# Kernel optimization log

Measured on AMD Instinct MI355X. Metric: run time of the kernel, lower is better.

The kernel has to match this reference:

```python
import jax, jax.numpy as jnp
import numpy as np

EPS = 1e-5      # F.layer_norm default eps
ALPHA = 0.08    # ALALLaDA blend coefficient


def setup_inputs() -> dict:
    key = jax.random.key(0)
    ks = jax.random.split(key, 6)
    B, S, D, K = 2, 2048, 2048, 8
    Fh = D // 4
    h_L = jax.random.normal(ks[0], (B, S, D), jnp.float32)
    # nonzero -> masked position (stands in for input_ids == 126336)
    mask = jax.random.randint(ks[1], (B, S), 0, 2).astype(jnp.int32)
    Wr = jax.random.normal(ks[2], (K, D), jnp.float32) / np.sqrt(D).astype(np.float32)
    br = jnp.zeros((K,), jnp.float32)
    W1 = jax.random.normal(ks[3], (K, D, Fh), jnp.float32) / np.sqrt(D).astype(np.float32)
    b1 = jnp.zeros((K, Fh), jnp.float32)
    W2 = jax.random.normal(ks[4], (K, Fh, D), jnp.float32) / np.sqrt(Fh).astype(np.float32)
    b2 = jnp.zeros((K, D), jnp.float32)
    return {"h_L": h_L, "mask": mask, "Wr": Wr, "br": br,
            "W1": W1, "b1": b1, "W2": W2, "b2": b2, "range_r": 8}


def _router_blend(h_L, Wr, br, W1, b1, W2, b2, mask, range_r):
    B, S, D = h_L.shape
    masked = mask != 0
    um = (~masked).astype(h_L.dtype)  # unmasked validity [B,S]
    # Per-token, per-expert outputs M[b,s,k,d]: Linear -> exact GELU -> Linear.
    pre = jnp.einsum('bsd,kdf->bskf', h_L, W1) + b1
    M = jnp.einsum('bskf,kfd->bskd', jax.nn.gelu(pre, approximate=False), W2) + b2
    # Routing weights at every position (softmax over K experts).
    w = jax.nn.softmax(jnp.einsum('bsd,kd->bsk', h_L, Wr) + br, axis=-1)
    # Accumulate weighted expert outputs over the +/-range_r neighbor window,
    # counting only unmasked neighbors. Fixed small loop over 2r offsets.
    num = jnp.zeros((B, S, D), h_L.dtype)
    cnt = jnp.zeros((B, S), h_L.dtype)
    for o in range(-range_r, range_r + 1):
        if o == 0:
            continue
        if o > 0:  # neighbor t = a + o: shift left, zero-pad tail
            Mo = jnp.pad(M[:, o:], ((0, 0), (0, o), (0, 0), (0, 0)))
            vo = jnp.pad(um[:, o:], ((0, 0), (0, o)))
        else:      # neighbor t = a + o (o<0): shift right, zero-pad head
            Mo = jnp.pad(M[:, :o], ((0, 0), (-o, 0), (0, 0), (0, 0)))
            vo = jnp.pad(um[:, :o], ((0, 0), (-o, 0)))
        num = num + vo[..., None] * jnp.einsum('bsk,bskd->bsd', w, Mo)
        cnt = cnt + vo
    has = cnt > 0
    mean = num / jnp.maximum(cnt, 1.0)[..., None]   # mean over valid neighbors
    # layer_norm over d_model, no affine
    mu = mean.mean(-1, keepdims=True)
    var = jnp.mean((mean - mu) ** 2, axis=-1, keepdims=True)
    ln = (mean - mu) / jnp.sqrt(var + EPS)
    # delta is written only at masked positions that had >=1 neighbor
    delta = jnp.where((masked & has)[..., None], ln, 0.0)
    return h_L + ALPHA * delta


def reference(h_L, mask, Wr, br, W1, b1, W2, b2, range_r):
    return _router_blend(h_L, Wr, br, W1, b1, W2, b2, mask, range_r)
```

## Files before the change

### kernel.cpp

```cpp
#include <hip/hip_runtime.h>
#include <hip/hip_bf16.h>
#include <math.h>


#define ALPHA 0.08f
#define EPS 1e-5f

typedef __attribute__((ext_vector_type(8))) __bf16 bf16x8;
typedef __attribute__((ext_vector_type(8))) short short8;
typedef __attribute__((ext_vector_type(4))) float f32x4;

__device__ __forceinline__ unsigned short f2bf(float f) {
  unsigned u = __float_as_uint(f);
  u += 0x7fffu + ((u >> 16) & 1u);
  return (unsigned short)(u >> 16);
}
__device__ __forceinline__ float bf2f(unsigned short b) {
  return __uint_as_float(((unsigned)b) << 16);
}

#define GLD16(gptr, lptr)                                                     \
  __builtin_amdgcn_global_load_lds(                                           \
      (const __attribute__((address_space(1))) void*)(gptr),                  \
      (__attribute__((address_space(3))) void*)(lptr), 16, 0, 0)

__device__ __forceinline__ int wave_incl_scan(int v, int lane) {
#pragma unroll
  for (int off = 1; off < 64; off <<= 1) {
    int t = __shfl_up(v, off);
    if (lane >= off) v += t;
  }
  return v;
}

__global__ __launch_bounds__(1024) void scan_kernel(
    const int* __restrict__ mask, const int* __restrict__ rptr,
    int* __restrict__ ru, int* __restrict__ unm_idx,
    int* __restrict__ msk_idx, int* __restrict__ pos2row,
    int* __restrict__ counts) {
  __shared__ int sru[4097];
  __shared__ int wsum[16];
  __shared__ int wsum2[17];
  const int tid = threadIdx.x;
  const int lane = tid & 63, wv = tid >> 6;
  const int t0 = tid * 4;
  const int4 m4 = *(const int4*)(mask + t0);
  int f[4];
  f[0] = (m4.x == 0); f[1] = (m4.y == 0); f[2] = (m4.z == 0); f[3] = (m4.w == 0);
  const int tsum = f[0] + f[1] + f[2] + f[3];
  const int isc = wave_incl_scan(tsum, lane);
  if (lane == 63) wsum[wv] = isc;
  __syncthreads();
  if (tid == 0) {
    int acc = 0;
#pragma unroll
    for (int i = 0; i < 16; ++i) { int v = wsum[i]; wsum[i] = acc; acc += v; }
    sru[4096] = acc;
    counts[0] = acc;
    ru[4096] = acc;
  }
  __syncthreads();
  int ex = wsum[wv] + isc - tsum;
#pragma unroll
  for (int j = 0; j < 4; ++j) {
    sru[t0 + j] = ex;
    ru[t0 + j] = ex;
    if (f[j]) unm_idx[ex] = t0 + j;
    ex += f[j];
  }
  __syncthreads();
  const int r = rptr[0];
  int mval[4] = {m4.x, m4.y, m4.z, m4.w};
  int g[4];
#pragma unroll
  for (int j = 0; j < 4; ++j) {
    const int t = t0 + j;
    const int s = t & 2047, tb = t & ~2047;
    const int lo = max(s - r, 0), hi = min(s + r, 2047);
    const int cnt = sru[tb + hi + 1] - sru[tb + lo];
    g[j] = (mval[j] != 0 && cnt > 0) ? 1 : 0;
  }
  const int tsum2 = g[0] + g[1] + g[2] + g[3];
  const int isc2 = wave_incl_scan(tsum2, lane);
  if (lane == 63) wsum2[wv] = isc2;
  __syncthreads();
  if (tid == 0) {
    int acc = 0;
#pragma unroll
    for (int i = 0; i < 16; ++i) { int v = wsum2[i]; wsum2[i] = acc; acc += v; }
    counts[1] = acc;
  }
  __syncthreads();
  int ex2 = wsum2[wv] + isc2 - tsum2;
#pragma unroll
  for (int j = 0; j < 4; ++j) {
    const int t = t0 + j;
    pos2row[t] = g[j] ? ex2 : -1;
    if (g[j]) msk_idx[ex2] = t;
    ex2 += g[j];
  }
}

__global__ void pack_h_kernel(const float* __restrict__ h,
                              const int* __restrict__ unm_idx,
                              const int* __restrict__ counts,
                              unsigned short* __restrict__ hbc) {
  const int i = blockIdx.x;
  if (i >= counts[0]) return;
  const int t = unm_idx[i];
  const int d0 = threadIdx.x * 8;
  const float4 x0 = *(const float4*)(h + (size_t)t * 2048 + d0);
  const float4 x1 = *(const float4*)(h + (size_t)t * 2048 + d0 + 4);
  short8 o;
  o[0] = (short)f2bf(x0.x); o[1] = (short)f2bf(x0.y);
  o[2] = (short)f2bf(x0.z); o[3] = (short)f2bf(x0.w);
  o[4] = (short)f2bf(x1.x); o[5] = (short)f2bf(x1.y);
  o[6] = (short)f2bf(x1.z); o[7] = (short)f2bf(x1.w);
  *(short8*)(hbc + (size_t)i * 2048 + d0) = o;
}

__global__ void transpose_pack_kernel(const float* __restrict__ src,
                                      unsigned short* __restrict__ dst,
                                      int R, int C, size_t dstStride,
                                      size_t dstExpStride) {
  __shared__ float tile[32][33];
  const int k = blockIdx.z;
  src += (size_t)k * (size_t)R * (size_t)C;
  dst += (size_t)k * dstExpStride;
  const int c0 = blockIdx.x * 32;
  const int r0 = blockIdx.y * 32;
  const int tx = threadIdx.x;
  const int ty = threadIdx.y;
#pragma unroll
  for (int i = 0; i < 4; ++i)
    tile[ty + 8 * i][tx] = src[(size_t)(r0 + ty + 8 * i) * C + (c0 + tx)];
  __syncthreads();
#pragma unroll
  for (int i = 0; i < 4; ++i) {
    const int c = c0 + ty + 8 * i;
    dst[(size_t)c * dstStride + (size_t)(r0 + tx)] = f2bf(tile[tx][ty + 8 * i]);
  }
}

__global__ void router_kernel(const float* __restrict__ h,
                              const float* __restrict__ Wr,
                              const float* __restrict__ br,
                              float* __restrict__ w) {
  const int a = blockIdx.x;
  const int tid = threadIdx.x;
  const int lane = tid & 63, wid = tid >> 6;
  const size_t base = (size_t)a * 2048;
  const int d0 = tid * 8;
  float hv[8];
  *(float4*)(hv) = *(const float4*)(h + base + d0);
  *(float4*)(hv + 4) = *(const float4*)(h + base + d0 + 4);
  float acc[8];
#pragma unroll
  for (int k = 0; k < 8; ++k) {
    float wvv[8];
    *(float4*)(wvv) = *(const float4*)(Wr + (size_t)k * 2048 + d0);
    *(float4*)(wvv + 4) = *(const float4*)(Wr + (size_t)k * 2048 + d0 + 4);
    float s = 0.f;
#pragma unroll
    for (int j = 0; j < 8; ++j) s += hv[j] * wvv[j];
    acc[k] = s;
  }
#pragma unroll
  for (int off = 32; off > 0; off >>= 1)
#pragma unroll
    for (int k = 0; k < 8; ++k) acc[k] += __shfl_down(acc[k], off);
  __shared__ float red[4][8];
  __shared__ float logits[8];
  if (lane == 0)
#pragma unroll
    for (int k = 0; k < 8; ++k) red[wid][k] = acc[k];
  __syncthreads();
  if (tid < 8)
    logits[tid] = red[0][tid] + red[1][tid] + red[2][tid] + red[3][tid] + br[tid];
  __syncthreads();
  if (tid == 0) {
    float mx = logits[0];
#pragma unroll
    for (int k = 1; k < 8; ++k) mx = fmaxf(mx, logits[k]);
    float e[8], se = 0.f;
#pragma unroll
    for (int k = 0; k < 8; ++k) {
      e[k] = expf(logits[k] - mx);
      se += e[k];
    }
    const float is = 1.f / se;
#pragma unroll
    for (int k = 0; k < 8; ++k) w[(size_t)a * 8 + k] = e[k] * is;
  }
}

template <int EPI>
__global__ __launch_bounds__(256, 2) void gemm_bt_kernel(
    const unsigned short* __restrict__ A, const unsigned short* __restrict__ Bt,
    float* __restrict__ Cf, unsigned short* __restrict__ Cb,
    const float* __restrict__ bias, const int* __restrict__ counts, int cidx,
    int N, int Kd) {
  const int Mlim = counts[cidx];
  const int bm = blockIdx.y * 128;
  if (bm >= Mlim) return;
  __shared__ __align__(16) unsigned short As[4096];
  __shared__ __align__(16) unsigned short Bs[4096];
  const int tid = threadIdx.x;
  const int lane = tid & 63;
  const int wid = tid >> 6;
  const int bn = blockIdx.x * 128;
  const int wr = wid >> 1;
  const int wc = wid & 1;

  f32x4 acc[4][4];
#pragma unroll
  for (int m = 0; m < 4; ++m)
#pragma unroll
    for (int n = 0; n < 4; ++n) acc[m][n] = (f32x4){0.f, 0.f, 0.f, 0.f};

  const int srow = wid * 16 + (lane >> 2);
  const int scol = (lane & 3) * 8;
  const unsigned short* gA0 = A + (size_t)(bm + srow) * Kd + scol;
  const unsigned short* gA1 = gA0 + (size_t)64 * Kd;
  const unsigned short* gB0 = Bt + (size_t)(bn + srow) * Kd + scol;
  const unsigned short* gB1 = gB0 + (size_t)64 * Kd;
  unsigned short* lA0 = As + wid * 512;
  unsigned short* lA1 = As + (wid + 4) * 512;
  unsigned short* lB0 = Bs + wid * 512;
  unsigned short* lB1 = Bs + (wid + 4) * 512;

  const int aoff = (wr * 64 + (lane & 15)) * 32 + (lane >> 4) * 8;
  const int boff = (wc * 64 + (lane & 15)) * 32 + (lane >> 4) * 8;

  for (int k0 = 0; k0 < Kd; k0 += 32) {
    __syncthreads();
    GLD16(gA0 + k0, lA0);
    GLD16(gA1 + k0, lA1);
    GLD16(gB0 + k0, lB0);
    GLD16(gB1 + k0, lB1);
    __syncthreads();
    bf16x8 af[4], bfr[4];
#pragma unroll
    for (int m = 0; m < 4; ++m)
      af[m] = __builtin_bit_cast(bf16x8, *(const short8*)(As + aoff + m * 512));
#pragma unroll
    for (int n = 0; n < 4; ++n)
      bfr[n] = __builtin_bit_cast(bf16x8, *(const short8*)(Bs + boff + n * 512));
#pragma unroll
    for (int m = 0; m < 4; ++m)
#pragma unroll
      for (int n = 0; n < 4; ++n)
        acc[m][n] = __builtin_amdgcn_mfma_f32_16x16x32_bf16(af[m], bfr[n],
                                                            acc[m][n], 0, 0, 0);
  }

  const int r0 = bm + wr * 64 + (lane >> 4) * 4;
  const int c0 = bn + wc * 64 + (lane & 15);
#pragma unroll
  for (int m = 0; m < 4; ++m) {
#pragma unroll
    for (int n = 0; n < 4; ++n) {
      const int col = c0 + n * 16;
#pragma unroll
      for (int i = 0; i < 4; ++i) {
        const int row = r0 + m * 16 + i;
        if (row >= Mlim) continue;
        const size_t off = (size_t)row * N + col;
        float v = acc[m][n][i];
        if (EPI == 1) {
          v += bias[col];
          v = 0.5f * v * (1.0f + erff(v * 0.70710678118654752f));
          Cb[off] = f2bf(v);
        } else {
          Cf[off] = v;
        }
      }
    }
  }
}

__global__ void window_kernel(const unsigned short* __restrict__ Act_c,
                              const float* __restrict__ w,
                              const int* __restrict__ msk_idx,
                              const int* __restrict__ ru,
                              const int* __restrict__ rptr,
                              const int* __restrict__ counts,
                              unsigned short* __restrict__ G_c) {
  const int i = blockIdx.y;
  if (i >= counts[1]) return;
  const int a = msk_idx[i];
  const int s = a & 2047;
  const int tb = a & ~2047;
  const int r = rptr[0];
  const int lo = max(s - r, 0), hi = min(s + r, 2047);
  const int jlo = ru[tb + lo], jhi = ru[tb + hi + 1];
  const int c = blockIdx.x * 2048 + threadIdx.x * 8;
  float acc[8] = {0.f, 0.f, 0.f, 0.f, 0.f, 0.f, 0.f, 0.f};
  for (int j = jlo; j < jhi; ++j) {
    const short8 v = *(const short8*)(Act_c + (size_t)j * 4096 + c);
#pragma unroll
    for (int jj = 0; jj < 8; ++jj) acc[jj] += bf2f((unsigned short)v[jj]);
  }
  const float wv = w[(size_t)a * 8 + (c >> 9)];
  short8 o8;
#pragma unroll
  for (int jj = 0; jj < 8; ++jj) o8[jj] = (short)f2bf(acc[jj] * wv);
  *(short8*)(G_c + (size_t)i * 4096 + c) = o8;
}

__global__ void final_kernel(const float* __restrict__ h,
                             const int* __restrict__ pos2row,
                             const float* __restrict__ w,
                             const float* __restrict__ b2,
                             const float* __restrict__ num_c,
                             const int* __restrict__ ru,
                             const int* __restrict__ rptr,
                             float* __restrict__ out) {
  const int a = blockIdx.x;
  const int tid = threadIdx.x;
  const int lane = tid & 63, wid = tid >> 6;
  const size_t base = (size_t)a * 2048;
  const int d0 = tid * 8;
  const int row = pos2row[a];
  if (row < 0) {
    const float4 x0 = *(const float4*)(h + base + d0);
    const float4 x1 = *(const float4*)(h + base + d0 + 4);
    *(float4*)(out + base + d0) = x0;
    *(float4*)(out + base + d0 + 4) = x1;
    return;
  }
  const int s = a & 2047;
  const int tb = a & ~2047;
  const int r = rptr[0];
  const int lo = max(s - r, 0), hi = min(s + r, 2047);
  const int cnt = ru[tb + hi + 1] - ru[tb + lo];
  float wk[8];
#pragma unroll
  for (int k = 0; k < 8; ++k) wk[k] = w[(size_t)a * 8 + k];
  const float cntf = (float)cnt;
  const float icnt = 1.0f / cntf;
  float mval[8];
  float s1 = 0.f, s2 = 0.f;
#pragma unroll
  for (int j = 0; j < 8; ++j) {
    const int d = d0 + j;
    float wb2 = 0.f;
#pragma unroll
    for (int k = 0; k < 8; ++k) wb2 += wk[k] * b2[(size_t)k * 2048 + d];
    const float v = (num_c[(size_t)row * 2048 + d] + cntf * wb2) * icnt;
    mval[j] = v;
    s1 += v;
    s2 += v * v;
  }
#pragma unroll
  for (int off = 32; off > 0; off >>= 1) {
    s1 += __shfl_down(s1, off);
    s2 += __shfl_down(s2, off);
  }
  __shared__ float red[8];
  if (lane == 0) {
    red[wid] = s1;
    red[4 + wid] = s2;
  }
  __syncthreads();
  const float S1 = red[0] + red[1] + red[2] + red[3];
  const float S2 = red[4] + red[5] + red[6] + red[7];
  const float mu = S1 * (1.0f / 2048.0f);
  const float var = S2 * (1.0f / 2048.0f) - mu * mu;
  const float rin = rsqrtf(var + EPS);
#pragma unroll
  for (int j = 0; j < 8; ++j) {
    const int d = d0 + j;
    out[base + d] = h[base + d] + ALPHA * ((mval[j] - mu) * rin);
  }
}

extern "C" void kernel_launch(void* const* d_in, const int* in_sizes, int n_in,
                              void* d_out, int out_size, void* d_ws,
                              size_t ws_size, hipStream_t stream) {
  const float* h = (const float*)d_in[0];
  const int* mask = (const int*)d_in[1];
  const float* Wr = (const float*)d_in[2];
  const float* br = (const float*)d_in[3];
  const float* W1 = (const float*)d_in[4];
  const float* b1 = (const float*)d_in[5];
  const float* W2 = (const float*)d_in[6];
  const float* b2 = (const float*)d_in[7];
  const int* rptr = (const int*)d_in[8];
  float* out = (float*)d_out;

  char* ws = (char*)d_ws;
  unsigned short* hbc = (unsigned short*)(ws + 0);
  unsigned short* B1t = (unsigned short*)(ws + 16777216);
  unsigned short* B2t = (unsigned short*)(ws + 33554432);
  unsigned short* Act_c = (unsigned short*)(ws + 50331648);
  unsigned short* G_c = (unsigned short*)(ws + 83886080);
  float* num_c = (float*)(ws + 50331648);
  float* wbuf = (float*)(ws + 117440512);
  int* ru = (int*)(ws + 117571584);
  int* unm_idx = ru + 4100;
  int* msk_idx = unm_idx + 4096;
  int* pos2row = msk_idx + 4096;
  int* counts = pos2row + 4096;

  scan_kernel<<<1, 1024, 0, stream>>>(mask, rptr, ru, unm_idx, msk_idx,
                                      pos2row, counts);
  pack_h_kernel<<<4096, 256, 0, stream>>>(h, unm_idx, counts, hbc);
  router_kernel<<<4096, 256, 0, stream>>>(h, Wr, br, wbuf);
  transpose_pack_kernel<<<dim3(16, 64, 8), dim3(32, 8), 0, stream>>>(
      W1, B1t, 2048, 512, 2048, (size_t)512 * 2048);
  transpose_pack_kernel<<<dim3(64, 16, 8), dim3(32, 8), 0, stream>>>(
      W2, B2t, 512, 2048, 4096, 512);
  gemm_bt_kernel<1><<<dim3(32, 32), 256, 0, stream>>>(
      hbc, B1t, nullptr, Act_c, b1, counts, 0, 4096, 2048);
  window_kernel<<<dim3(2, 4096), 256, 0, stream>>>(Act_c, wbuf, msk_idx, ru,
                                                   rptr, counts, G_c);
  gemm_bt_kernel<0><<<dim3(16, 32), 256, 0, stream>>>(
      G_c, B2t, num_c, nullptr, nullptr, counts, 1, 2048, 4096);
  final_kernel<<<4096, 256, 0, stream>>>(h, pos2row, wbuf, b2, num_c, ru,
                                         rptr, out);
}
```

Before: 375.5 us.

## Multi-buffer GEMM LDS loads with 4-stage pipeline and fuse pack with router

The GEMM main loop moves from a single LDS buffer with two barriers per k-step to a 4-deep ring of buffers. Three stages are prefetched with global_load_lds, and explicit vmcnt waits let loads overlap MFMA compute. Separately, the bf16 packing of unmasked rows is merged into the router kernel so h is read once instead of twice, saving one launch. LDS per block grows to 64KB, which may limit occupancy relative to the launch_bounds(256,2) target.

New measurement: 346.7 us. 7.6% less time.

```diff
diff --git a/kernel.cpp b/kernel.cpp
--- a/kernel.cpp
+++ b/kernel.cpp
@@ -101,22 +101,66 @@
   }
 }
 
-__global__ void pack_h_kernel(const float* __restrict__ h,
-                              const int* __restrict__ unm_idx,
-                              const int* __restrict__ counts,
-                              unsigned short* __restrict__ hbc) {
-  const int i = blockIdx.x;
-  if (i >= counts[0]) return;
-  const int t = unm_idx[i];
-  const int d0 = threadIdx.x * 8;
-  const float4 x0 = *(const float4*)(h + (size_t)t * 2048 + d0);
-  const float4 x1 = *(const float4*)(h + (size_t)t * 2048 + d0 + 4);
-  short8 o;
-  o[0] = (short)f2bf(x0.x); o[1] = (short)f2bf(x0.y);
-  o[2] = (short)f2bf(x0.z); o[3] = (short)f2bf(x0.w);
-  o[4] = (short)f2bf(x1.x); o[5] = (short)f2bf(x1.y);
-  o[6] = (short)f2bf(x1.z); o[7] = (short)f2bf(x1.w);
-  *(short8*)(hbc + (size_t)i * 2048 + d0) = o;
+__global__ void packrouter_kernel(const float* __restrict__ h,
+                                  const int* __restrict__ mask,
+                                  const int* __restrict__ ru,
+                                  const float* __restrict__ Wr,
+                                  const float* __restrict__ br,
+                                  float* __restrict__ w,
+                                  unsigned short* __restrict__ hbc) {
+  const int a = blockIdx.x;
+  const int tid = threadIdx.x;
+  const int lane = tid & 63, wid = tid >> 6;
+  const size_t base = (size_t)a * 2048;
+  const int d0 = tid * 8;
+  float hv[8];
+  *(float4*)(hv) = *(const float4*)(h + base + d0);
+  *(float4*)(hv + 4) = *(const float4*)(h + base + d0 + 4);
+  float acc[8];
+#pragma unroll
+  for (int k = 0; k < 8; ++k) {
+    float wvv[8];
+    *(float4*)(wvv) = *(const float4*)(Wr + (size_t)k * 2048 + d0);
+    *(float4*)(wvv + 4) = *(const float4*)(Wr + (size_t)k * 2048 + d0 + 4);
+    float s = 0.f;
+#pragma unroll
+    for (int j = 0; j < 8; ++j) s += hv[j] * wvv[j];
+    acc[k] = s;
+  }
+#pragma unroll
+  for (int off = 32; off > 0; off >>= 1)
+#pragma unroll
+    for (int k = 0; k < 8; ++k) acc[k] += __shfl_down(acc[k], off);
+  __shared__ float red[4][8];
+  __shared__ float logits[8];
+  if (lane == 0)
+#pragma unroll
+    for (int k = 0; k < 8; ++k) red[wid][k] = acc[k];
+  __syncthreads();
+  if (tid < 8)
+    logits[tid] = red[0][tid] + red[1][tid] + red[2][tid] + red[3][tid] + br[tid];
+  __syncthreads();
+  if (tid == 0) {
+    float mx = logits[0];
+#pragma unroll
+    for (int k = 1; k < 8; ++k) mx = fmaxf(mx, logits[k]);
+    float e[8], se = 0.f;
+#pragma unroll
+    for (int k = 0; k < 8; ++k) {
+      e[k] = expf(logits[k] - mx);
+      se += e[k];
+    }
+    const float is = 1.f / se;
+#pragma unroll
+    for (int k = 0; k < 8; ++k) w[(size_t)a * 8 + k] = e[k] * is;
+  }
+  if (mask[a] == 0) {
+    const int i = ru[a];
+    short8 o;
+#pragma unroll
+    for (int j = 0; j < 8; ++j) o[j] = (short)f2bf(hv[j]);
+    *(short8*)(hbc + (size_t)i * 2048 + d0) = o;
+  }
 }
 
 __global__ void transpose_pack_kernel(const float* __restrict__ src,
@@ -142,58 +186,6 @@
   }
 }
 
-__global__ void router_kernel(const float* __restrict__ h,
-                              const float* __restrict__ Wr,
-                              const float* __restrict__ br,
-                              float* __restrict__ w) {
-  const int a = blockIdx.x;
-  const int tid = threadIdx.x;
-  const int lane = tid & 63, wid = tid >> 6;
-  const size_t base = (size_t)a * 2048;
-  const int d0 = tid * 8;
-  float hv[8];
-  *(float4*)(hv) = *(const float4*)(h + base + d0);
-  *(float4*)(hv + 4) = *(const float4*)(h + base + d0 + 4);
-  float acc[8];
-#pragma unroll
-  for (int k = 0; k < 8; ++k) {
-    float wvv[8];
-    *(float4*)(wvv) = *(const float4*)(Wr + (size_t)k * 2048 + d0);
-    *(float4*)(wvv + 4) = *(const float4*)(Wr + (size_t)k * 2048 + d0 + 4);
-    float s = 0.f;
-#pragma unroll
-    for (int j = 0; j < 8; ++j) s += hv[j] * wvv[j];
-    acc[k] = s;
-  }
-#pragma unroll
-  for (int off = 32; off > 0; off >>= 1)
-#pragma unroll
-    for (int k = 0; k < 8; ++k) acc[k] += __shfl_down(acc[k], off);
-  __shared__ float red[4][8];
-  __shared__ float logits[8];
-  if (lane == 0)
-#pragma unroll
-    for (int k = 0; k < 8; ++k) red[wid][k] = acc[k];
-  __syncthreads();
-  if (tid < 8)
-    logits[tid] = red[0][tid] + red[1][tid] + red[2][tid] + red[3][tid] + br[tid];
-  __syncthreads();
-  if (tid == 0) {
-    float mx = logits[0];
-#pragma unroll
-    for (int k = 1; k < 8; ++k) mx = fmaxf(mx, logits[k]);
-    float e[8], se = 0.f;
-#pragma unroll
-    for (int k = 0; k < 8; ++k) {
-      e[k] = expf(logits[k] - mx);
-      se += e[k];
-    }
-    const float is = 1.f / se;
-#pragma unroll
-    for (int k = 0; k < 8; ++k) w[(size_t)a * 8 + k] = e[k] * is;
-  }
-}
-
 template <int EPI>
 __global__ __launch_bounds__(256, 2) void gemm_bt_kernel(
     const unsigned short* __restrict__ A, const unsigned short* __restrict__ Bt,
@@ -203,8 +195,7 @@
   const int Mlim = counts[cidx];
   const int bm = blockIdx.y * 128;
   if (bm >= Mlim) return;
-  __shared__ __align__(16) unsigned short As[4096];
-  __shared__ __align__(16) unsigned short Bs[4096];
+  __shared__ __align__(16) unsigned short L[4][8192];
   const int tid = threadIdx.x;
   const int lane = tid & 63;
   const int wid = tid >> 6;
@@ -224,35 +215,68 @@
   const unsigned short* gA1 = gA0 + (size_t)64 * Kd;
   const unsigned short* gB0 = Bt + (size_t)(bn + srow) * Kd + scol;
   const unsigned short* gB1 = gB0 + (size_t)64 * Kd;
-  unsigned short* lA0 = As + wid * 512;
-  unsigned short* lA1 = As + (wid + 4) * 512;
-  unsigned short* lB0 = Bs + wid * 512;
-  unsigned short* lB1 = Bs + (wid + 4) * 512;
 
   const int aoff = (wr * 64 + (lane & 15)) * 32 + (lane >> 4) * 8;
   const int boff = (wc * 64 + (lane & 15)) * 32 + (lane >> 4) * 8;
 
-  for (int k0 = 0; k0 < Kd; k0 += 32) {
-    __syncthreads();
-    GLD16(gA0 + k0, lA0);
-    GLD16(gA1 + k0, lA1);
-    GLD16(gB0 + k0, lB0);
-    GLD16(gB1 + k0, lB1);
-    __syncthreads();
-    bf16x8 af[4], bfr[4];
-#pragma unroll
-    for (int m = 0; m < 4; ++m)
-      af[m] = __builtin_bit_cast(bf16x8, *(const short8*)(As + aoff + m * 512));
-#pragma unroll
-    for (int n = 0; n < 4; ++n)
-      bfr[n] = __builtin_bit_cast(bf16x8, *(const short8*)(Bs + boff + n * 512));
-#pragma unroll
-    for (int m = 0; m < 4; ++m)
-#pragma unroll
-      for (int n = 0; n < 4; ++n)
-        acc[m][n] = __builtin_amdgcn_mfma_f32_16x16x32_bf16(af[m], bfr[n],
-                                                            acc[m][n], 0, 0, 0);
-  }
+#define STAGE(buf, t)                                                         \
+  {                                                                           \
+    const int k0_ = (t) << 5;                                                 \
+    unsigned short* la_ = &L[(buf)][0] + wid * 512;                           \
+    unsigned short* lb_ = &L[(buf)][4096] + wid * 512;                        \
+    GLD16(gA0 + k0_, la_);                                                    \
+    GLD16(gA1 + k0_, la_ + 2048);                                             \
+    GLD16(gB0 + k0_, lb_);                                                    \
+    GLD16(gB1 + k0_, lb_ + 2048);                                             \
+  }
+
+#define COMPUTE(buf)                                                          \
+  {                                                                           \
+    const unsigned short* As_ = &L[(buf)][0];                                 \
+    const unsigned short* Bs_ = &L[(buf)][4096];                              \
+    bf16x8 af[4], bfr[4];                                                     \
+    _Pragma("unroll") for (int m = 0; m < 4; ++m) af[m] =                     \
+        __builtin_bit_cast(bf16x8, *(const short8*)(As_ + aoff + m * 512));   \
+    _Pragma("unroll") for (int n = 0; n < 4; ++n) bfr[n] =                    \
+        __builtin_bit_cast(bf16x8, *(const short8*)(Bs_ + boff + n * 512));   \
+    _Pragma("unroll") for (int m = 0; m < 4; ++m)                             \
+        _Pragma("unroll") for (int n = 0; n < 4; ++n) acc[m][n] =             \
+            __builtin_amdgcn_mfma_f32_16x16x32_bf16(af[m], bfr[n],            \
+                                                    acc[m][n], 0, 0, 0);      \
+  }
+
+  const int nt = Kd >> 5;
+  STAGE(0, 0);
+  STAGE(1, 1);
+  STAGE(2, 2);
+#pragma unroll 1
+  for (int t = 0; t < nt - 3; ++t) {
+    asm volatile("s_waitcnt vmcnt(8)" ::: "memory");
+    __builtin_amdgcn_s_barrier();
+    __builtin_amdgcn_sched_barrier(0);
+    STAGE((t + 3) & 3, t + 3);
+    COMPUTE(t & 3);
+  }
+  {
+    asm volatile("s_waitcnt vmcnt(8)" ::: "memory");
+    __builtin_amdgcn_s_barrier();
+    __builtin_amdgcn_sched_barrier(0);
+    COMPUTE((nt - 3) & 3);
+  }
+  {
+    asm volatile("s_waitcnt vmcnt(4)" ::: "memory");
+    __builtin_amdgcn_s_barrier();
+    __builtin_amdgcn_sched_barrier(0);
+    COMPUTE((nt - 2) & 3);
+  }
+  {
+    asm volatile("s_waitcnt vmcnt(0)" ::: "memory");
+    __builtin_amdgcn_s_barrier();
+    __builtin_amdgcn_sched_barrier(0);
+    COMPUTE((nt - 1) & 3);
+  }
+#undef STAGE
+#undef COMPUTE
 
   const int r0 = bm + wr * 64 + (lane >> 4) * 4;
   const int c0 = bn + wc * 64 + (lane & 15);
@@ -405,8 +429,7 @@
 
   scan_kernel<<<1, 1024, 0, stream>>>(mask, rptr, ru, unm_idx, msk_idx,
                                       pos2row, counts);
-  pack_h_kernel<<<4096, 256, 0, stream>>>(h, unm_idx, counts, hbc);
-  router_kernel<<<4096, 256, 0, stream>>>(h, Wr, br, wbuf);
+  packrouter_kernel<<<4096, 256, 0, stream>>>(h, mask, ru, Wr, br, wbuf, hbc);
   transpose_pack_kernel<<<dim3(16, 64, 8), dim3(32, 8), 0, stream>>>(
       W1, B1t, 2048, 512, 2048, (size_t)512 * 2048);
   transpose_pack_kernel<<<dim3(64, 16, 8), dim3(32, 8), 0, stream>>>(
```
